# Performance work log

Hardware: AMD Instinct MI355X
Metric: run time of the kernel (lower is better)

The kernel has to match this reference:

```python
import jax, jax.numpy as jnp
import numpy as np

VOCAB = 50257
EMB = 1024
H = 1024
LAYERS = 2
B = 64
S = 512


def gru_cell(x, h, w_ih, w_hh, b_ih, b_hh):
    # PyTorch GRUCell math. x:[B,in], h:[B,H], w_ih:[3H,in], w_hh:[3H,H]
    gi = x @ w_ih.T + b_ih            # [B,3H]
    gh = h @ w_hh.T + b_hh            # [B,3H]
    i_r, i_z, i_n = jnp.split(gi, 3, axis=1)
    h_r, h_z, h_n = jnp.split(gh, 3, axis=1)
    r = jax.nn.sigmoid(i_r + h_r)
    z = jax.nn.sigmoid(i_z + h_z)
    n = jnp.tanh(i_n + r * h_n)
    return (1.0 - z) * n + z * h


def setup_inputs() -> dict:
    key = jax.random.key(0)
    ks = jax.random.split(key, 16)
    s = 0.02
    inp = {
        "input_step": jax.random.randint(ks[0], (1, B), 0, VOCAB),
        "last_hidden": jax.random.normal(ks[1], (LAYERS, B, H), jnp.float32),
        "encoder_outputs": jax.random.normal(ks[2], (S, B, H), jnp.float32),
        "emb_table": jax.random.normal(ks[3], (VOCAB, EMB), jnp.float32) * s,
        "w_ih0": jax.random.normal(ks[4], (3 * H, EMB), jnp.float32) * s,
        "w_hh0": jax.random.normal(ks[5], (3 * H, H), jnp.float32) * s,
        "b_ih0": jnp.zeros((3 * H,), jnp.float32),
        "b_hh0": jnp.zeros((3 * H,), jnp.float32),
        "w_ih1": jax.random.normal(ks[6], (3 * H, H), jnp.float32) * s,
        "w_hh1": jax.random.normal(ks[7], (3 * H, H), jnp.float32) * s,
        "b_ih1": jnp.zeros((3 * H,), jnp.float32),
        "b_hh1": jnp.zeros((3 * H,), jnp.float32),
        "concat_w": jax.random.normal(ks[8], (H, 2 * H), jnp.float32) * s,
        "concat_b": jnp.zeros((H,), jnp.float32),
        "out_w": jax.random.normal(ks[9], (VOCAB, H), jnp.float32) * s,
        "out_b": jnp.zeros((VOCAB,), jnp.float32),
    }
    return inp


def reference(input_step, last_hidden, encoder_outputs, emb_table,
              w_ih0, w_hh0, b_ih0, b_hh0, w_ih1, w_hh1, b_ih1, b_hh1,
              concat_w, concat_b, out_w, out_b):
    # embedding (dropout=0 / eval mode)
    x = emb_table[input_step[0]]                       # [B,EMB]
    # 2-layer GRU, single time step
    h0 = gru_cell(x, last_hidden[0], w_ih0, w_hh0, b_ih0, b_hh0)   # [B,H]
    h1 = gru_cell(h0, last_hidden[1], w_ih1, w_hh1, b_ih1, b_hh1)  # [B,H]
    rnn_output = h1                                    # [B,H]
    hidden = jnp.stack([h0, h1], axis=0)               # [LAYERS,B,H]
    # Luong dot attention: scores [S,B] -> softmax over S per batch
    scores = jnp.einsum('bh,sbh->bs', rnn_output, encoder_outputs)  # [B,S]
    attn = jax.nn.softmax(scores, axis=1)              # [B,S]
    context = jnp.einsum('bs,sbh->bh', attn, encoder_outputs)       # [B,H]
    concat_in = jnp.concatenate([rnn_output, context], axis=1)      # [B,2H]
    concat_out = jnp.tanh(concat_in @ concat_w.T + concat_b)        # [B,H]
    logits = concat_out @ out_w.T + out_b              # [B,VOCAB]
    output = jax.nn.softmax(logits, axis=1)
    return (output, hidden)
```

## Files before the change

kernel.cpp:

```cpp
#include <hip/hip_runtime.h>
#include <hip/hip_bf16.h>
#include <math.h>

#define VOCAB 50257
#define EMB   1024
#define HID   1024
#define BATCH 64
#define SEQ   512
#define LOGITS_LD 50304
#define SCH   16
#define NCHUNK (SEQ / SCH)
#define NSLAB 786

typedef __attribute__((ext_vector_type(8))) short bf16x8;
typedef __attribute__((ext_vector_type(4))) float f32x4;

typedef const __attribute__((address_space(1))) unsigned int gu32_t;
typedef __attribute__((address_space(3))) unsigned int lu32_t;

__device__ inline short f2bf(float x) {
    __hip_bfloat16 h = __float2bfloat16(x);
    return *reinterpret_cast<short*>(&h);
}

__device__ inline bf16x8 cvt8(const float4& a, const float4& b) {
    bf16x8 r;
    r[0] = f2bf(a.x); r[1] = f2bf(a.y); r[2] = f2bf(a.z); r[3] = f2bf(a.w);
    r[4] = f2bf(b.x); r[5] = f2bf(b.y); r[6] = f2bf(b.z); r[7] = f2bf(b.w);
    return r;
}

struct Prob {
    const void*  A;
    const int*   gidx;
    const float* W;
    const float* bias;
    float*       C;
    int N, K, ldc;
};

template <int KSLEN, int ADD_BIAS, int A_BF16>
__global__ __launch_bounds__(128, 2) void gemm_k(Prob p0, Prob p1, Prob p2)
{
    Prob P = (blockIdx.y == 0) ? p0 : ((blockIdx.y == 1) ? p1 : p2);

    const int lane = threadIdx.x & 63;
    const int wv   = threadIdx.x >> 6;
    const int rowi = lane & 15;
    const int kgi  = lane >> 4;
    const int col  = blockIdx.x * 32 + wv * 16 + rowi;
    const int wcol = min(col, P.N - 1);
    const int kbase = blockIdx.z * KSLEN + kgi * 8;

    const float* wp = P.W + (size_t)wcol * P.K + kbase;

    const float*  af[4];
    const ushort* ah[4];
#pragma unroll
    for (int mt = 0; mt < 4; ++mt) {
        int r  = rowi + mt * 16;
        int ar = P.gidx ? P.gidx[r] : r;
        af[mt] = (const float*) P.A + (size_t)ar * P.K + kbase;
        ah[mt] = (const ushort*)P.A + (size_t)ar * P.K + kbase;
    }

    f32x4 acc[4] = {};

    float4 wa0, wb0, wa1, wb1;
    bf16x8 h0b[4], h1b[4];
    float4 f0a[4], f0b[4], f1a[4], f1b[4];

    wa0 = *(const float4*)(wp);
    wb0 = *(const float4*)(wp + 4);
#pragma unroll
    for (int mt = 0; mt < 4; ++mt) {
        if (A_BF16) h0b[mt] = *(const bf16x8*)(ah[mt]);
        else { f0a[mt] = *(const float4*)(af[mt]); f0b[mt] = *(const float4*)(af[mt] + 4); }
    }
    wa1 = *(const float4*)(wp + 32);
    wb1 = *(const float4*)(wp + 36);
#pragma unroll
    for (int mt = 0; mt < 4; ++mt) {
        if (A_BF16) h1b[mt] = *(const bf16x8*)(ah[mt] + 32);
        else { f1a[mt] = *(const float4*)(af[mt] + 32); f1b[mt] = *(const float4*)(af[mt] + 36); }
    }

#pragma unroll
    for (int ks = 0; ks < KSLEN; ks += 64) {
        {
            float4 nwa = {}, nwb = {};
            bf16x8 nh[4] = {};
            float4 nfa[4] = {}, nfb[4] = {};
            if (ks + 64 < KSLEN) {
                nwa = *(const float4*)(wp + ks + 64);
                nwb = *(const float4*)(wp + ks + 68);
#pragma unroll
                for (int mt = 0; mt < 4; ++mt) {
                    if (A_BF16) nh[mt] = *(const bf16x8*)(ah[mt] + ks + 64);
                    else { nfa[mt] = *(const float4*)(af[mt] + ks + 64);
                           nfb[mt] = *(const float4*)(af[mt] + ks + 68); }
                }
            }
            bf16x8 b = cvt8(wa0, wb0);
#pragma unroll
            for (int mt = 0; mt < 4; ++mt) {
                bf16x8 a;
                if (A_BF16) a = h0b[mt]; else a = cvt8(f0a[mt], f0b[mt]);
                acc[mt] = __builtin_amdgcn_mfma_f32_16x16x32_bf16(a, b, acc[mt], 0, 0, 0);
            }
            wa0 = nwa; wb0 = nwb;
#pragma unroll
            for (int mt = 0; mt < 4; ++mt) {
                if (A_BF16) h0b[mt] = nh[mt];
                else { f0a[mt] = nfa[mt]; f0b[mt] = nfb[mt]; }
            }
        }
        {
            float4 nwa = {}, nwb = {};
            bf16x8 nh[4] = {};
            float4 nfa[4] = {}, nfb[4] = {};
            if (ks + 96 < KSLEN) {
                nwa = *(const float4*)(wp + ks + 96);
                nwb = *(const float4*)(wp + ks + 100);
#pragma unroll
                for (int mt = 0; mt < 4; ++mt) {
                    if (A_BF16) nh[mt] = *(const bf16x8*)(ah[mt] + ks + 96);
                    else { nfa[mt] = *(const float4*)(af[mt] + ks + 96);
                           nfb[mt] = *(const float4*)(af[mt] + ks + 100); }
                }
            }
            bf16x8 b = cvt8(wa1, wb1);
#pragma unroll
            for (int mt = 0; mt < 4; ++mt) {
                bf16x8 a;
                if (A_BF16) a = h1b[mt]; else a = cvt8(f1a[mt], f1b[mt]);
                acc[mt] = __builtin_amdgcn_mfma_f32_16x16x32_bf16(a, b, acc[mt], 0, 0, 0);
            }
            wa1 = nwa; wb1 = nwb;
#pragma unroll
            for (int mt = 0; mt < 4; ++mt) {
                if (A_BF16) h1b[mt] = nh[mt];
                else { f1a[mt] = nfa[mt]; f1b[mt] = nfb[mt]; }
            }
        }
    }

    if (col < P.N) {
        float bv = ADD_BIAS ? P.bias[col] : 0.0f;
        float* C = P.C + (size_t)blockIdx.z * 64 * P.ldc;
#pragma unroll
        for (int mt = 0; mt < 4; ++mt)
#pragma unroll
            for (int r = 0; r < 4; ++r) {
                int row = mt * 16 + kgi * 4 + r;
                C[(size_t)row * P.ldc + col] = acc[mt][r] + bv;
            }
    }
}

__global__ __launch_bounds__(256) void logits_pers_k(
    const ushort* __restrict__ co_bf, const float* __restrict__ W,
    const float* __restrict__ bias, float* __restrict__ logits,
    float* __restrict__ pmax, float* __restrict__ psum, int* __restrict__ ctr)
{
    __shared__ ushort co_s[64 * 1024];
    __shared__ float smax[4][64], ssum[4][64];
    __shared__ int slab_s;

    const int tid  = threadIdx.x;
    const int lane = tid & 63;
    const int wv   = tid >> 6;
    const int rowi = lane & 15;
    const int kgi  = lane >> 4;

#pragma unroll
    for (int rnd = 0; rnd < 32; ++rnd) {
        int o     = rnd * 4096 + tid * 16;
        int row   = o >> 11;
        int inner = o & 2047;
        int src   = (row << 11) + (inner ^ ((row & 7) << 4));
        __builtin_amdgcn_global_load_lds(
            (gu32_t*)((const char*)co_bf + src),
            (lu32_t*)(((char*)co_s) + rnd * 4096 + wv * 1024), 16, 0, 0);
    }
    __syncthreads();

    const int rloc = wv * 16 + rowi;

    while (true) {
        if (tid == 0) slab_s = atomicAdd(ctr, 1);
        __syncthreads();
        const int slab = slab_s;
        if (slab >= NSLAB) break;

        const int nblk = slab * 64;
        const int wrow = min(nblk + rloc, VOCAB - 1);
        const float* wp = W + (size_t)wrow * 1024 + kgi * 8;

        f32x4 acc[4] = {};
        float4 wa0 = *(const float4*)(wp);
        float4 wb0 = *(const float4*)(wp + 4);
        float4 wa1 = *(const float4*)(wp + 32);
        float4 wb1 = *(const float4*)(wp + 36);

#pragma unroll
        for (int s = 0; s < 32; s += 2) {
            float4 na0 = {}, nb0 = {}, na1 = {}, nb1 = {};
            if (s + 2 < 32) {
                na0 = *(const float4*)(wp + (s + 2) * 32);
                nb0 = *(const float4*)(wp + (s + 2) * 32 + 4);
            }
            if (s + 3 < 32) {
                na1 = *(const float4*)(wp + (s + 3) * 32);
                nb1 = *(const float4*)(wp + (s + 3) * 32 + 4);
            }
            {
                bf16x8 wf = cvt8(wa0, wb0);
                const int kb = s * 64 + kgi * 16;
#pragma unroll
                for (int cf = 0; cf < 4; ++cf) {
                    int row = cf * 16 + rowi;
                    const char* p = ((const char*)co_s) + row * 2048 +
                                    (kb ^ ((row & 7) << 4));
                    bf16x8 a = *(const bf16x8*)p;
                    acc[cf] = __builtin_amdgcn_mfma_f32_16x16x32_bf16(wf, a, acc[cf], 0, 0, 0);
                }
            }
            {
                bf16x8 wf = cvt8(wa1, wb1);
                const int kb = (s + 1) * 64 + kgi * 16;
#pragma unroll
                for (int cf = 0; cf < 4; ++cf) {
                    int row = cf * 16 + rowi;
                    const char* p = ((const char*)co_s) + row * 2048 +
                                    (kb ^ ((row & 7) << 4));
                    bf16x8 a = *(const bf16x8*)p;
                    acc[cf] = __builtin_amdgcn_mfma_f32_16x16x32_bf16(wf, a, acc[cf], 0, 0, 0);
                }
            }
            wa0 = na0; wb0 = nb0; wa1 = na1; wb1 = nb1;
        }

        const int nb = nblk + wv * 16 + kgi * 4;
        float vals[4][4];
#pragma unroll
        for (int cf = 0; cf < 4; ++cf) {
            int b = cf * 16 + rowi;
#pragma unroll
            for (int r = 0; r < 4; ++r)
                vals[cf][r] = acc[cf][r] + bias[min(nb + r, VOCAB - 1)];
            float4 o = {vals[cf][0], vals[cf][1], vals[cf][2], vals[cf][3]};
            *(float4*)(logits + (size_t)b * LOGITS_LD + nb) = o;
        }
#pragma unroll
        for (int cf = 0; cf < 4; ++cf) {
            float m = -INFINITY;
#pragma unroll
            for (int r = 0; r < 4; ++r)
                if (nb + r < VOCAB) m = fmaxf(m, vals[cf][r]);
            m = fmaxf(m, __shfl_xor(m, 16));
            m = fmaxf(m, __shfl_xor(m, 32));
            float sm = 0.0f;
#pragma unroll
            for (int r = 0; r < 4; ++r)
                if (nb + r < VOCAB) sm += expf(vals[cf][r] - m);
            sm += __shfl_xor(sm, 16);
            sm += __shfl_xor(sm, 32);
            if (kgi == 0) { smax[wv][cf * 16 + rowi] = m; ssum[wv][cf * 16 + rowi] = sm; }
        }
        __syncthreads();
        if (tid < 64) {
            float m = fmaxf(fmaxf(smax[0][tid], smax[1][tid]),
                            fmaxf(smax[2][tid], smax[3][tid]));
            float t = 0.0f;
#pragma unroll
            for (int w = 0; w < 4; ++w) {
                float sw = ssum[w][tid];
                t += (sw > 0.0f) ? sw * expf(smax[w][tid] - m) : 0.0f;
            }
            pmax[(size_t)slab * 64 + tid] = m;
            psum[(size_t)slab * 64 + tid] = t;
        }
        __syncthreads();
    }
}

__global__ __launch_bounds__(256) void vfinal_k(
    const float* __restrict__ pmax, const float* __restrict__ psum,
    float* __restrict__ gm, float* __restrict__ ginv)
{
    const int b = blockIdx.x;
    __shared__ float red[4];
    float m = -INFINITY;
    for (int s = threadIdx.x; s < NSLAB; s += 256)
        m = fmaxf(m, pmax[(size_t)s * 64 + b]);
    for (int off = 32; off; off >>= 1) m = fmaxf(m, __shfl_xor(m, off));
    int wv = threadIdx.x >> 6, lane = threadIdx.x & 63;
    if (lane == 0) red[wv] = m;
    __syncthreads();
    m = fmaxf(fmaxf(red[0], red[1]), fmaxf(red[2], red[3]));
    float t = 0.0f;
    for (int s = threadIdx.x; s < NSLAB; s += 256)
        t += psum[(size_t)s * 64 + b] * expf(pmax[(size_t)s * 64 + b] - m);
    for (int off = 32; off; off >>= 1) t += __shfl_xor(t, off);
    __syncthreads();
    if (lane == 0) red[wv] = t;
    __syncthreads();
    if (threadIdx.x == 0) { gm[b] = m; ginv[b] = 1.0f / (red[0] + red[1] + red[2] + red[3]); }
}

template <int NZI, int NZH>
__global__ __launch_bounds__(256) void gru_gate_k(
    const float* __restrict__ pgi, const float* __restrict__ pgh,
    const float* __restrict__ b_ih, const float* __restrict__ b_hh,
    const float* __restrict__ hprev, float* __restrict__ out_hidden,
    float* __restrict__ h_out, float* __restrict__ ci)
{
    int i = blockIdx.x * 256 + threadIdx.x;
    int b = i >> 10, j = i & 1023;
    size_t base = (size_t)b * 3072 + j;
    float ir = b_ih[j], iz = b_ih[j + 1024], in_ = b_ih[j + 2048];
    float hr = b_hh[j], hz = b_hh[j + 1024], hn  = b_hh[j + 2048];
#pragma unroll
    for (int z = 0; z < NZI; ++z) {
        size_t o = (size_t)z * 64 * 3072 + base;
        ir += pgi[o]; iz += pgi[o + 1024]; in_ += pgi[o + 2048];
    }
#pragma unroll
    for (int z = 0; z < NZH; ++z) {
        size_t o = (size_t)z * 64 * 3072 + base;
        hr += pgh[o]; hz += pgh[o + 1024]; hn  += pgh[o + 2048];
    }
    float r = 1.0f / (1.0f + expf(-(ir + hr)));
    float z = 1.0f / (1.0f + expf(-(iz + hz)));
    float n = tanhf(in_ + r * hn);
    float v = (1.0f - z) * n + z * hprev[i];
    out_hidden[i] = v;
    if (h_out) h_out[i] = v;
    if (ci)    ci[(size_t)b * 2048 + j] = v;
}

__global__ __launch_bounds__(256) void attn_fused_k(
    const float* __restrict__ h1, const float* __restrict__ enc,
    float* __restrict__ pctx, float* __restrict__ pm, float* __restrict__ ps)
{
    const int b = blockIdx.y, ck = blockIdx.x;
    __shared__ float hs[HID];
    __shared__ float es[SCH][HID];
    __shared__ float sc[SCH];
    const int tid = threadIdx.x, wv = tid >> 6, lane = tid & 63;

    ((float4*)hs)[tid] = ((const float4*)(h1 + (size_t)b * HID))[tid];
    const float* ebase = enc + ((size_t)(ck * SCH) * BATCH + b) * HID;
#pragma unroll
    for (int i = 0; i < SCH; ++i) {
        int idx = tid + i * 256;
        int r = idx >> 8, c = idx & 255;
        ((float4*)es[r])[c] = ((const float4*)(ebase + (size_t)r * BATCH * HID))[c];
    }
    __syncthreads();

#pragma unroll
    for (int i = 0; i < 4; ++i) {
        int r = wv * 4 + i;
        float acc = 0.0f;
#pragma unroll
        for (int seg = 0; seg < 4; ++seg) {
            float4 ev = ((const float4*)es[r])[lane + seg * 64];
            float4 hv = ((const float4*)hs)[lane + seg * 64];
            acc += ev.x * hv.x + ev.y * hv.y + ev.z * hv.z + ev.w * hv.w;
        }
        for (int off = 32; off; off >>= 1) acc += __shfl_down(acc, off);
        if (lane == 0) sc[r] = acc;
    }
    __syncthreads();

    float m = sc[0];
#pragma unroll
    for (int s = 1; s < SCH; ++s) m = fmaxf(m, sc[s]);
    float p[SCH];
    float sum = 0.0f;
#pragma unroll
    for (int s = 0; s < SCH; ++s) { p[s] = expf(sc[s] - m); sum += p[s]; }

    float4 cacc = {0.0f, 0.0f, 0.0f, 0.0f};
#pragma unroll
    for (int s = 0; s < SCH; ++s) {
        float4 ev = ((const float4*)es[s])[tid];
        cacc.x += p[s] * ev.x; cacc.y += p[s] * ev.y;
        cacc.z += p[s] * ev.z; cacc.w += p[s] * ev.w;
    }
    ((float4*)(pctx + ((size_t)ck * BATCH + b) * HID))[tid] = cacc;
    if (tid == 0) { pm[b * NCHUNK + ck] = m; ps[b * NCHUNK + ck] = sum; }
}

__global__ __launch_bounds__(256) void attn_comb_k(
    const float* __restrict__ pctx, const float* __restrict__ pm,
    const float* __restrict__ ps, float* __restrict__ ci)
{
    const int b = blockIdx.x, tid = threadIdx.x;
    float m = -INFINITY;
#pragma unroll
    for (int c = 0; c < NCHUNK; ++c) m = fmaxf(m, pm[b * NCHUNK + c]);
    float w[NCHUNK]; float tot = 0.0f;
#pragma unroll
    for (int c = 0; c < NCHUNK; ++c) {
        w[c] = expf(pm[b * NCHUNK + c] - m);
        tot += ps[b * NCHUNK + c] * w[c];
    }
    float inv = 1.0f / tot;
    float4 acc = {0.0f, 0.0f, 0.0f, 0.0f};
#pragma unroll
    for (int c = 0; c < NCHUNK; ++c) {
        float4 v = ((const float4*)(pctx + ((size_t)c * BATCH + b) * HID))[tid];
        acc.x += w[c] * v.x; acc.y += w[c] * v.y;
        acc.z += w[c] * v.z; acc.w += w[c] * v.w;
    }
    float4 o = {acc.x * inv, acc.y * inv, acc.z * inv, acc.w * inv};
    ((float4*)(ci + (size_t)b * 2048 + 1024))[tid] = o;
}

__global__ __launch_bounds__(256) void concat_comb_k(
    const float* __restrict__ pco, const float* __restrict__ bias,
    ushort* __restrict__ co_bf, int* __restrict__ ctr)
{
    if (blockIdx.x == 0 && threadIdx.x == 0) *ctr = 0;
    int i = blockIdx.x * 256 + threadIdx.x;
    int j = i & 1023;
    float v = bias[j];
#pragma unroll
    for (int z = 0; z < 8; ++z) v += pco[(size_t)z * 65536 + i];
    co_bf[i] = (ushort)f2bf(tanhf(v));
}

__global__ __launch_bounds__(256) void softmax_v_k(
    const float* __restrict__ logits, const float* __restrict__ gm,
    const float* __restrict__ ginv, float* __restrict__ out)
{
    int b = blockIdx.y;
    float m = gm[b], inv = ginv[b];
    int v = blockIdx.x * 1024 + threadIdx.x * 4;
    if (v + 3 < VOCAB) {
        float4 lv = *reinterpret_cast<const float4*>(logits + (size_t)b * LOGITS_LD + v);
        float4 o;
        o.x = expf(lv.x - m) * inv; o.y = expf(lv.y - m) * inv;
        o.z = expf(lv.z - m) * inv; o.w = expf(lv.w - m) * inv;
        *reinterpret_cast<float4*>(out + (size_t)b * VOCAB + v) = o;
    } else {
        for (int k = 0; k < 4 && v + k < VOCAB; ++k)
            out[(size_t)b * VOCAB + v + k] = expf(logits[(size_t)b * LOGITS_LD + v + k] - m) * inv;
    }
}

extern "C" void kernel_launch(void* const* d_in, const int* in_sizes, int n_in,
                              void* d_out, int out_size, void* d_ws, size_t ws_size,
                              hipStream_t stream)
{
    const int*   input_step  = (const int*)  d_in[0];
    const float* last_hidden = (const float*)d_in[1];
    const float* enc         = (const float*)d_in[2];
    const float* emb         = (const float*)d_in[3];
    const float* w_ih0       = (const float*)d_in[4];
    const float* w_hh0       = (const float*)d_in[5];
    const float* b_ih0       = (const float*)d_in[6];
    const float* b_hh0       = (const float*)d_in[7];
    const float* w_ih1       = (const float*)d_in[8];
    const float* w_hh1       = (const float*)d_in[9];
    const float* b_ih1       = (const float*)d_in[10];
    const float* b_hh1       = (const float*)d_in[11];
    const float* concat_w    = (const float*)d_in[12];
    const float* concat_b    = (const float*)d_in[13];
    const float* out_w       = (const float*)d_in[14];
    const float* out_b       = (const float*)d_in[15];

    float* out = (float*)d_out;
    float* out_probs  = out;
    float* out_hidden = out + (size_t)BATCH * VOCAB;

    float* ws   = (float*)d_ws;
    float* big  = ws;
    float* pgi0 = big;
    float* pgh0 = big + 786432;
    float* pgh1 = big + 1572864;
    float* pgi1 = big;
    float* pctx = big;
    float* pco  = big;
    float* logits = ws + 2359296;
    float* ci   = logits + (size_t)64 * LOGITS_LD;
    float* h0   = ci + 131072;
    float* pm   = h0 + 65536;
    float* ps   = pm + 2048;
    float* pmax = ps + 2048;
    float* psum = pmax + 50304;
    float* gm   = psum + 50304;
    float* ginv = gm + 64;
    int*   ctr  = (int*)(ginv + 64);
    ushort* co_bf = (ushort*)(ginv + 64 + 16);

    Prob P0 = { emb,         input_step, w_ih0, nullptr, pgi0, 3 * HID, EMB, 3 * HID };
    Prob P1 = { last_hidden, nullptr,    w_hh0, nullptr, pgh0, 3 * HID, HID, 3 * HID };
    Prob P2 = { last_hidden + 64 * HID, nullptr, w_hh1, nullptr, pgh1, 3 * HID, HID, 3 * HID };

    gemm_k<256, 0, 0><<<dim3(96, 3, 4), 128, 0, stream>>>(P0, P1, P2);

    gru_gate_k<4, 4><<<256, 256, 0, stream>>>(pgi0, pgh0, b_ih0, b_hh0, last_hidden,
                                              out_hidden, h0, nullptr);

    Prob PB = { h0, nullptr, w_ih1, nullptr, pgi1, 3 * HID, HID, 3 * HID };
    gemm_k<128, 0, 0><<<dim3(96, 1, 8), 128, 0, stream>>>(PB, PB, PB);

    gru_gate_k<8, 4><<<256, 256, 0, stream>>>(pgi1, pgh1, b_ih1, b_hh1,
                                              last_hidden + 64 * HID,
                                              out_hidden + 64 * HID, nullptr, ci);

    attn_fused_k<<<dim3(NCHUNK, BATCH), 256, 0, stream>>>(
        out_hidden + 64 * HID, enc, pctx, pm, ps);
    attn_comb_k<<<BATCH, 256, 0, stream>>>(pctx, pm, ps, ci);

    Prob PC = { ci, nullptr, concat_w, nullptr, pco, HID, 2 * HID, HID };
    gemm_k<256, 0, 0><<<dim3(32, 1, 8), 128, 0, stream>>>(PC, PC, PC);
    concat_comb_k<<<256, 256, 0, stream>>>(pco, concat_b, co_bf, ctr);

    logits_pers_k<<<256, 256, 0, stream>>>(co_bf, out_w, out_b, logits, pmax, psum, ctr);

    vfinal_k<<<BATCH, 256, 0, stream>>>(pmax, psum, gm, ginv);
    softmax_v_k<<<dim3((VOCAB + 1023) / 1024, BATCH), 256, 0, stream>>>(
        logits, gm, ginv, out_probs);
}
```

Before: 194.4 us.

## Stage logits weight tiles through LDS with triple-buffered async global_load_lds

Weight rows for each 64-row output slab are now loaded asynchronously into a triple-buffered shared-memory ring using global_load_lds. Previously they were loaded per thread into registers with a two-step software prefetch. The loop waits on vmcnt counters and uses two barriers per K-chunk so loads overlap with MFMA work and global accesses are more coalesced. The cost is extra LDS usage, which may lower occupancy alongside the 128KB co_s buffer, plus per-iteration barrier overhead.

```diff
diff --git a/kernel.cpp b/kernel.cpp
--- a/kernel.cpp
+++ b/kernel.cpp
@@ -164,8 +164,9 @@
     float* __restrict__ pmax, float* __restrict__ psum, int* __restrict__ ctr)
 {
     __shared__ ushort co_s[64 * 1024];
-    __shared__ float smax[4][64], ssum[4][64];
-    __shared__ int slab_s;
+    __shared__ float  w_s[3][2048];
+    __shared__ float  smax[4][64], ssum[4][64];
+    __shared__ int    slab_sh;
 
     const int tid  = threadIdx.x;
     const int lane = tid & 63;
@@ -183,65 +184,73 @@
             (gu32_t*)((const char*)co_bf + src),
             (lu32_t*)(((char*)co_s) + rnd * 4096 + wv * 1024), 16, 0, 0);
     }
-    __syncthreads();
+    asm volatile("s_waitcnt vmcnt(0)" ::: "memory");
+    __builtin_amdgcn_s_barrier();
 
     const int rloc = wv * 16 + rowi;
+    const int wswz = (rloc & 7) << 4;
+
+    const int rowA = tid >> 3;
+    const int rowB = 32 + (tid >> 3);
+    const int swzA = ((((tid & 7) << 4) ^ ((rowA & 7) << 4)) >> 2);
+    const int swzB = ((((tid & 7) << 4) ^ ((rowB & 7) << 4)) >> 2);
 
     while (true) {
-        if (tid == 0) slab_s = atomicAdd(ctr, 1);
+        if (tid == 0) slab_sh = atomicAdd(ctr, 1);
         __syncthreads();
-        const int slab = slab_s;
+        const int slab = slab_sh;
+        __syncthreads();
         if (slab >= NSLAB) break;
 
-        const int nblk = slab * 64;
-        const int wrow = min(nblk + rloc, VOCAB - 1);
-        const float* wp = W + (size_t)wrow * 1024 + kgi * 8;
+        const int r0 = slab * 64;
+        const size_t sA = (size_t)min(r0 + rowA, VOCAB - 1) * 1024 + swzA;
+        const size_t sB = (size_t)min(r0 + rowB, VOCAB - 1) * 1024 + swzB;
+
+#define STAGE_CHUNK(bufidx, c) do {                                          \
+        __builtin_amdgcn_global_load_lds((gu32_t*)(W + sA + (c) * 32),       \
+            (lu32_t*)(((char*)w_s) + (bufidx) * 8192 + wv * 1024), 16, 0, 0);\
+        __builtin_amdgcn_global_load_lds((gu32_t*)(W + sB + (c) * 32),       \
+            (lu32_t*)(((char*)w_s) + (bufidx) * 8192 + 4096 + wv * 1024),    \
+            16, 0, 0);                                                       \
+    } while (0)
+
+        STAGE_CHUNK(0, 0);
+        STAGE_CHUNK(1, 1);
+        STAGE_CHUNK(2, 2);
 
         f32x4 acc[4] = {};
-        float4 wa0 = *(const float4*)(wp);
-        float4 wb0 = *(const float4*)(wp + 4);
-        float4 wa1 = *(const float4*)(wp + 32);
-        float4 wb1 = *(const float4*)(wp + 36);
-
-#pragma unroll
-        for (int s = 0; s < 32; s += 2) {
-            float4 na0 = {}, nb0 = {}, na1 = {}, nb1 = {};
-            if (s + 2 < 32) {
-                na0 = *(const float4*)(wp + (s + 2) * 32);
-                nb0 = *(const float4*)(wp + (s + 2) * 32 + 4);
-            }
-            if (s + 3 < 32) {
-                na1 = *(const float4*)(wp + (s + 3) * 32);
-                nb1 = *(const float4*)(wp + (s + 3) * 32 + 4);
-            }
-            {
-                bf16x8 wf = cvt8(wa0, wb0);
-                const int kb = s * 64 + kgi * 16;
-#pragma unroll
-                for (int cf = 0; cf < 4; ++cf) {
-                    int row = cf * 16 + rowi;
-                    const char* p = ((const char*)co_s) + row * 2048 +
-                                    (kb ^ ((row & 7) << 4));
-                    bf16x8 a = *(const bf16x8*)p;
-                    acc[cf] = __builtin_amdgcn_mfma_f32_16x16x32_bf16(wf, a, acc[cf], 0, 0, 0);
-                }
-            }
-            {
-                bf16x8 wf = cvt8(wa1, wb1);
-                const int kb = (s + 1) * 64 + kgi * 16;
-#pragma unroll
-                for (int cf = 0; cf < 4; ++cf) {
-                    int row = cf * 16 + rowi;
-                    const char* p = ((const char*)co_s) + row * 2048 +
-                                    (kb ^ ((row & 7) << 4));
-                    bf16x8 a = *(const bf16x8*)p;
-                    acc[cf] = __builtin_amdgcn_mfma_f32_16x16x32_bf16(wf, a, acc[cf], 0, 0, 0);
-                }
-            }
-            wa0 = na0; wb0 = nb0; wa1 = na1; wb1 = nb1;
-        }
-
-        const int nb = nblk + wv * 16 + kgi * 4;
+
+#pragma unroll
+        for (int t = 0; t < 32; ++t) {
+            if (t < 30)       asm volatile("s_waitcnt vmcnt(4)" ::: "memory");
+            else if (t == 30) asm volatile("s_waitcnt vmcnt(2)" ::: "memory");
+            else              asm volatile("s_waitcnt vmcnt(0)" ::: "memory");
+            __builtin_amdgcn_sched_barrier(0);
+            __builtin_amdgcn_s_barrier();
+            __builtin_amdgcn_sched_barrier(0);
+
+            const char* wbase = ((const char*)w_s) + (t % 3) * 8192 + rloc * 128;
+            float4 wa = *(const float4*)(wbase + ((kgi * 32) ^ wswz));
+            float4 wb = *(const float4*)(wbase + ((kgi * 32 + 16) ^ wswz));
+            bf16x8 wf = cvt8(wa, wb);
+#pragma unroll
+            for (int cf = 0; cf < 4; ++cf) {
+                int row = cf * 16 + rowi;
+                const char* p = ((const char*)co_s) + row * 2048 +
+                                ((t * 64 + kgi * 16) ^ ((row & 7) << 4));
+                bf16x8 a = *(const bf16x8*)p;
+                acc[cf] = __builtin_amdgcn_mfma_f32_16x16x32_bf16(wf, a, acc[cf], 0, 0, 0);
+            }
+
+            asm volatile("s_waitcnt lgkmcnt(0)" ::: "memory");
+            __builtin_amdgcn_sched_barrier(0);
+            __builtin_amdgcn_s_barrier();
+            __builtin_amdgcn_sched_barrier(0);
+            if (t + 3 < 32) STAGE_CHUNK(t % 3, t + 3);
+        }
+#undef STAGE_CHUNK
+
+        const int nb = r0 + wv * 16 + kgi * 4;
         float vals[4][4];
 #pragma unroll
         for (int cf = 0; cf < 4; ++cf) {
```

Measured after the change: 199.1 us. 1.02x slower.

## Restructure logits GEMM: register-resident activations, LDS double-buffered weight panels

Applied to the files above, without the earlier changes.

The vocab projection kernel now keeps the bf16 concat activations in registers per wave instead of in a 128KB LDS copy. Weight rows are staged cooperatively through double-buffered 16-row LDS panels, converted to bf16 on write, with coalesced row loads. An online max/sum replaces the cross-wave shared reduction. LDS use drops, so the launch bounds and grid double to two blocks per CU. The cost is heavy register pressure (32 bf16x8 fragments) and extra barriers per panel.

```diff
diff --git a/kernel.cpp b/kernel.cpp
--- a/kernel.cpp
+++ b/kernel.cpp
@@ -15,9 +15,6 @@
 typedef __attribute__((ext_vector_type(8))) short bf16x8;
 typedef __attribute__((ext_vector_type(4))) float f32x4;
 
-typedef const __attribute__((address_space(1))) unsigned int gu32_t;
-typedef __attribute__((address_space(3))) unsigned int lu32_t;
-
 __device__ inline short f2bf(float x) {
     __hip_bfloat16 h = __float2bfloat16(x);
     return *reinterpret_cast<short*>(&h);
@@ -158,128 +155,124 @@
     }
 }
 
-__global__ __launch_bounds__(256) void logits_pers_k(
+__device__ __forceinline__ void issue_panel(const float* __restrict__ W, int r0,
+                                            int p, int tid, float4 (&stg)[16])
+{
+#pragma unroll
+    for (int i = 0; i < 16; ++i) {
+        int grow = min(r0 + p * 16 + i, VOCAB - 1);
+        stg[i] = *(const float4*)(W + (size_t)grow * 1024 + tid * 4);
+    }
+}
+
+__device__ __forceinline__ void write_panel(ushort* buf, int tid,
+                                            const float4 (&stg)[16])
+{
+#pragma unroll
+    for (int i = 0; i < 16; ++i) {
+        unsigned lo = (unsigned)(unsigned short)f2bf(stg[i].x) |
+                      ((unsigned)(unsigned short)f2bf(stg[i].y) << 16);
+        unsigned hi = (unsigned)(unsigned short)f2bf(stg[i].z) |
+                      ((unsigned)(unsigned short)f2bf(stg[i].w) << 16);
+        uint2 u = {lo, hi};
+        *(uint2*)((char*)buf + i * 2048 + ((tid * 8) ^ ((i & 7) << 4))) = u;
+    }
+}
+
+__global__ __launch_bounds__(256, 2) void logits_panel_k(
     const ushort* __restrict__ co_bf, const float* __restrict__ W,
     const float* __restrict__ bias, float* __restrict__ logits,
     float* __restrict__ pmax, float* __restrict__ psum, int* __restrict__ ctr)
 {
-    __shared__ ushort co_s[64 * 1024];
-    __shared__ float smax[4][64], ssum[4][64];
-    __shared__ int slab_s;
+    __shared__ ushort wp_s[2][16 * 1024];
+    __shared__ int slab_sh;
 
     const int tid  = threadIdx.x;
     const int lane = tid & 63;
     const int wv   = tid >> 6;
     const int rowi = lane & 15;
     const int kgi  = lane >> 4;
-
-#pragma unroll
-    for (int rnd = 0; rnd < 32; ++rnd) {
-        int o     = rnd * 4096 + tid * 16;
-        int row   = o >> 11;
-        int inner = o & 2047;
-        int src   = (row << 11) + (inner ^ ((row & 7) << 4));
-        __builtin_amdgcn_global_load_lds(
-            (gu32_t*)((const char*)co_bf + src),
-            (lu32_t*)(((char*)co_s) + rnd * 4096 + wv * 1024), 16, 0, 0);
-    }
-    __syncthreads();
-
-    const int rloc = wv * 16 + rowi;
+    const int wswz = (rowi & 7) << 4;
+
+    bf16x8 cob[32];
+    {
+        const ushort* cp = co_bf + (size_t)(wv * 16 + rowi) * 1024 + kgi * 8;
+#pragma unroll
+        for (int s = 0; s < 32; ++s)
+            cob[s] = *(const bf16x8*)(cp + s * 32);
+    }
 
     while (true) {
-        if (tid == 0) slab_s = atomicAdd(ctr, 1);
+        if (tid == 0) slab_sh = atomicAdd(ctr, 1);
         __syncthreads();
-        const int slab = slab_s;
+        const int slab = slab_sh;
+        __syncthreads();
         if (slab >= NSLAB) break;
-
-        const int nblk = slab * 64;
-        const int wrow = min(nblk + rloc, VOCAB - 1);
-        const float* wp = W + (size_t)wrow * 1024 + kgi * 8;
-
-        f32x4 acc[4] = {};
-        float4 wa0 = *(const float4*)(wp);
-        float4 wb0 = *(const float4*)(wp + 4);
-        float4 wa1 = *(const float4*)(wp + 32);
-        float4 wb1 = *(const float4*)(wp + 36);
-
-#pragma unroll
-        for (int s = 0; s < 32; s += 2) {
-            float4 na0 = {}, nb0 = {}, na1 = {}, nb1 = {};
-            if (s + 2 < 32) {
-                na0 = *(const float4*)(wp + (s + 2) * 32);
-                nb0 = *(const float4*)(wp + (s + 2) * 32 + 4);
-            }
-            if (s + 3 < 32) {
-                na1 = *(const float4*)(wp + (s + 3) * 32);
-                nb1 = *(const float4*)(wp + (s + 3) * 32 + 4);
-            }
-            {
-                bf16x8 wf = cvt8(wa0, wb0);
-                const int kb = s * 64 + kgi * 16;
-#pragma unroll
-                for (int cf = 0; cf < 4; ++cf) {
-                    int row = cf * 16 + rowi;
-                    const char* p = ((const char*)co_s) + row * 2048 +
-                                    (kb ^ ((row & 7) << 4));
-                    bf16x8 a = *(const bf16x8*)p;
-                    acc[cf] = __builtin_amdgcn_mfma_f32_16x16x32_bf16(wf, a, acc[cf], 0, 0, 0);
-                }
-            }
-            {
-                bf16x8 wf = cvt8(wa1, wb1);
-                const int kb = (s + 1) * 64 + kgi * 16;
-#pragma unroll
-                for (int cf = 0; cf < 4; ++cf) {
-                    int row = cf * 16 + rowi;
-                    const char* p = ((const char*)co_s) + row * 2048 +
-                                    (kb ^ ((row & 7) << 4));
-                    bf16x8 a = *(const bf16x8*)p;
-                    acc[cf] = __builtin_amdgcn_mfma_f32_16x16x32_bf16(wf, a, acc[cf], 0, 0, 0);
-                }
-            }
-            wa0 = na0; wb0 = nb0; wa1 = na1; wb1 = nb1;
+        const int r0 = slab * 64;
+
+        float4 stg[16];
+
+        issue_panel(W, r0, 0, tid, stg);
+        write_panel(wp_s[0], tid, stg);
+        issue_panel(W, r0, 1, tid, stg);
+        asm volatile("s_waitcnt lgkmcnt(0)" ::: "memory");
+        __builtin_amdgcn_s_barrier();
+
+        float m_run = -INFINITY, s_run = 0.0f;
+
+#pragma unroll
+        for (int p = 0; p < 4; ++p) {
+            f32x4 acc = {};
+#pragma unroll
+            for (int ks = 0; ks < 32; ++ks) {
+                bf16x8 wf = *(const bf16x8*)((const char*)wp_s[p & 1] +
+                            rowi * 2048 + ((ks * 64 + kgi * 16) ^ wswz));
+                acc = __builtin_amdgcn_mfma_f32_16x16x32_bf16(wf, cob[ks], acc, 0, 0, 0);
+            }
+
+            const int vb = r0 + p * 16 + kgi * 4;
+            const int bq = wv * 16 + rowi;
+            float vals[4];
+            if (vb + 3 < VOCAB) {
+                float4 bv = *(const float4*)(bias + vb);
+                vals[0] = acc[0] + bv.x; vals[1] = acc[1] + bv.y;
+                vals[2] = acc[2] + bv.z; vals[3] = acc[3] + bv.w;
+            } else {
+#pragma unroll
+                for (int r = 0; r < 4; ++r)
+                    vals[r] = acc[r] + bias[min(vb + r, VOCAB - 1)];
+            }
+            float4 o = {vals[0], vals[1], vals[2], vals[3]};
+            *(float4*)(logits + (size_t)bq * LOGITS_LD + vb) = o;
+
+            float pmv = -INFINITY;
+#pragma unroll
+            for (int r = 0; r < 4; ++r)
+                if (vb + r < VOCAB) pmv = fmaxf(pmv, vals[r]);
+            pmv = fmaxf(pmv, __shfl_xor(pmv, 16));
+            pmv = fmaxf(pmv, __shfl_xor(pmv, 32));
+            float sp = 0.0f;
+#pragma unroll
+            for (int r = 0; r < 4; ++r)
+                if (vb + r < VOCAB) sp += expf(vals[r] - pmv);
+            sp += __shfl_xor(sp, 16);
+            sp += __shfl_xor(sp, 32);
+            float nm = fmaxf(m_run, pmv);
+            s_run = s_run * expf(m_run - nm) +
+                    ((pmv == -INFINITY) ? 0.0f : sp * expf(pmv - nm));
+            m_run = nm;
+
+            if (p < 3) {
+                write_panel(wp_s[(p + 1) & 1], tid, stg);
+                if (p < 2) issue_panel(W, r0, p + 2, tid, stg);
+                asm volatile("s_waitcnt lgkmcnt(0)" ::: "memory");
+                __builtin_amdgcn_s_barrier();
+            }
         }
 
-        const int nb = nblk + wv * 16 + kgi * 4;
-        float vals[4][4];
-#pragma unroll
-        for (int cf = 0; cf < 4; ++cf) {
-            int b = cf * 16 + rowi;
-#pragma unroll
-            for (int r = 0; r < 4; ++r)
-                vals[cf][r] = acc[cf][r] + bias[min(nb + r, VOCAB - 1)];
-            float4 o = {vals[cf][0], vals[cf][1], vals[cf][2], vals[cf][3]};
-            *(float4*)(logits + (size_t)b * LOGITS_LD + nb) = o;
-        }
-#pragma unroll
-        for (int cf = 0; cf < 4; ++cf) {
-            float m = -INFINITY;
-#pragma unroll
-            for (int r = 0; r < 4; ++r)
-                if (nb + r < VOCAB) m = fmaxf(m, vals[cf][r]);
-            m = fmaxf(m, __shfl_xor(m, 16));
-            m = fmaxf(m, __shfl_xor(m, 32));
-            float sm = 0.0f;
-#pragma unroll
-            for (int r = 0; r < 4; ++r)
-                if (nb + r < VOCAB) sm += expf(vals[cf][r] - m);
-            sm += __shfl_xor(sm, 16);
-            sm += __shfl_xor(sm, 32);
-            if (kgi == 0) { smax[wv][cf * 16 + rowi] = m; ssum[wv][cf * 16 + rowi] = sm; }
-        }
-        __syncthreads();
-        if (tid < 64) {
-            float m = fmaxf(fmaxf(smax[0][tid], smax[1][tid]),
-                            fmaxf(smax[2][tid], smax[3][tid]));
-            float t = 0.0f;
-#pragma unroll
-            for (int w = 0; w < 4; ++w) {
-                float sw = ssum[w][tid];
-                t += (sw > 0.0f) ? sw * expf(smax[w][tid] - m) : 0.0f;
-            }
-            pmax[(size_t)slab * 64 + tid] = m;
-            psum[(size_t)slab * 64 + tid] = t;
+        if (kgi == 0) {
+            pmax[(size_t)slab * 64 + wv * 16 + rowi] = m_run;
+            psum[(size_t)slab * 64 + wv * 16 + rowi] = s_run;
         }
         __syncthreads();
     }
@@ -521,7 +514,7 @@
     gemm_k<256, 0, 0><<<dim3(32, 1, 8), 128, 0, stream>>>(PC, PC, PC);
     concat_comb_k<<<256, 256, 0, stream>>>(pco, concat_b, co_bf, ctr);
 
-    logits_pers_k<<<256, 256, 0, stream>>>(co_bf, out_w, out_b, logits, pmax, psum, ctr);
+    logits_panel_k<<<512, 256, 0, stream>>>(co_bf, out_w, out_b, logits, pmax, psum, ctr);
 
     vfinal_k<<<BATCH, 256, 0, stream>>>(pmax, psum, gm, ginv);
     softmax_v_k<<<dim3((VOCAB + 1023) / 1024, BATCH), 256, 0, stream>>>(
```

After: 172.7 us (median of 2 runs). 11.2% less time.
